# Kernel optimization log

Measured on AMD Instinct MI355X. Metric: run time of the kernel, lower is better.

The kernel has to match this reference:

```python
import jax, jax.numpy as jnp
import numpy as np

B, N, DIM_S, E = 128, 2048, 128, 128


def _xavier(key, shape):
    fan_out, fan_in = shape[0], shape[1]
    limit = float(np.sqrt(6.0 / (fan_in + fan_out)))
    return jax.random.uniform(key, shape, jnp.float32, -limit, limit)


def setup_inputs() -> dict:
    key = jax.random.key(0)
    ks = jax.random.split(key, 14)
    return {
        "instance": jax.random.normal(ks[0], (B, N, DIM_S), jnp.float32),
        # conv1d kernel-size-1 embeds == per-node linear layers [out, in]
        "W_s": _xavier(ks[1], (E, DIM_S)),
        "b_s": jnp.zeros((E,), jnp.float32),
        "W_a": _xavier(ks[2], (E, E)),
        "b_a": jnp.zeros((E,), jnp.float32),
        "v_a": jax.random.normal(ks[3], (E,), jnp.float32),
        "W_c": _xavier(ks[4], (E, 2 * E)),
        "b_c": jnp.zeros((E,), jnp.float32),
        "v_c": jax.random.normal(ks[5], (E,), jnp.float32),
        "W1": _xavier(ks[6], (E, E)),
        "b1": jnp.zeros((E,), jnp.float32),
        "W2": _xavier(ks[7], (1, E)),
        "b2": jnp.zeros((1,), jnp.float32),
    }


def reference(instance, W_s, b_s, W_a, b_a, v_a, W_c, b_c, v_c, W1, b1, W2, b2):
    # project_s: conv1d k=1 == linear over feature dim. [B,N,E]
    proj = jnp.einsum("bns,es->bne", instance, W_s) + b_s
    # first additive-attention score: v_a . tanh(w_a(proj))  -> [B,N]
    u_t = jnp.einsum("bne,e->bn", jnp.tanh(jnp.einsum("bne,fe->bnf", proj, W_a) + b_a), v_a)
    a_t = jax.nn.softmax(u_t, axis=1)  # softmax over nodes
    c_t = a_t[:, :, None] * proj  # [B,N,E]
    hidden_2 = jnp.concatenate([proj, c_t], axis=2)  # [B,N,2E]
    u_t_2 = jnp.einsum("bne,e->bn", jnp.tanh(jnp.einsum("bnf,ef->bne", hidden_2, W_c) + b_c), v_c)
    prob = jax.nn.softmax(u_t_2, axis=1)  # [B,N]
    h_i = jnp.einsum("bn,bne->be", prob, proj)  # weighted sum -> [B,E]
    out1 = jax.nn.relu(h_i @ W1.T + b1)  # [B,E]
    v = (out1 @ W2.T + b2)[:, 0]  # [B]
    return v
```

## Files before the change

kernel.cpp:

```cpp
#include <hip/hip_runtime.h>
#include <hip/hip_bf16.h>

typedef _Float16 half8 __attribute__((ext_vector_type(8)));
typedef _Float16 half4v __attribute__((ext_vector_type(4)));
typedef float f32x4 __attribute__((ext_vector_type(4)));

#define SWZ(byte, r) ((unsigned)(byte) ^ ((((unsigned)(r)) & 7u) << 4))

constexpr int Bb = 128;
constexpr int Nn = 2048;
constexpr int Ee = 128;

constexpr size_t OFF_W    = 0;
constexpr size_t OFF_PROJ = 131072;
constexpr size_t OFF_UT   = OFF_PROJ + (size_t)Bb * Nn * Ee * 2;
constexpr size_t OFF_UT2  = OFF_UT   + (size_t)Bb * Nn * 4;
constexpr size_t OFF_HP   = OFF_UT2  + (size_t)Bb * Nn * 4;

__device__ __forceinline__ void cp16(void* lds, const void* g) {
    __builtin_amdgcn_global_load_lds(
        (const __attribute__((address_space(1))) unsigned int*)g,
        (__attribute__((address_space(3))) unsigned int*)lds, 16, 0, 0);
}

__device__ __forceinline__ float fast_tanh(float x) {
    float e = __expf(2.0f * x);
    return 1.0f - 2.0f * __builtin_amdgcn_rcpf(e + 1.0f);
}

__global__ __launch_bounds__(256) void k_prep(const float* __restrict__ Ws,
                                              const float* __restrict__ Wa,
                                              const float* __restrict__ Wc,
                                              char* __restrict__ wdst)
{
    int id = blockIdx.x * 256 + threadIdx.x;
    for (int i = id; i < 65536; i += 64 * 256) {
        int mat = i >> 14;
        int rem = i & 16383;
        int r = rem >> 7, c = rem & 127;
        float v;
        if      (mat == 0) v = Ws[r * 128 + c];
        else if (mat == 1) v = Wa[r * 128 + c];
        else if (mat == 2) v = Wc[r * 256 + c];
        else               v = Wc[r * 256 + 128 + c];
        unsigned off = SWZ((unsigned)((r * 128 + c) * 2), r);
        *reinterpret_cast<_Float16*>(wdst + (size_t)mat * 32768 + off) = (_Float16)v;
    }
}

__global__ __launch_bounds__(256) void k_pass1(const float* __restrict__ inst,
                                               const char* __restrict__ wtiles,
                                               const float* __restrict__ bs,
                                               const float* __restrict__ ba,
                                               const float* __restrict__ va,
                                               char* __restrict__ projg,
                                               float* __restrict__ ut)
{
    __shared__ _Float16 ldsW[2 * 16384];
    __shared__ _Float16 buf[8192];

    const int tid  = threadIdx.x;
    const int lane = tid & 63;
    const int w    = tid >> 6;
    const int l15  = lane & 15;
    const int kg   = lane >> 4;
    const int arow = w * 16 + l15;

    #pragma unroll
    for (int i = 0; i < 16; ++i) {
        unsigned o = (unsigned)((i * 256 + tid) * 16);
        cp16((char*)ldsW + o, wtiles + o);
    }

    const size_t tile0 = (size_t)blockIdx.x * 8;
    float4 v[8];
    {
        const float* src = inst + tile0 * 64 * 128;
        #pragma unroll
        for (int i = 0; i < 8; ++i)
            v[i] = *reinterpret_cast<const float4*>(src + (size_t)(i * 256 + tid) * 4);
    }

    for (int it = 0; it < 8; ++it) {
        const size_t row0 = (tile0 + it) * 64;

        #pragma unroll
        for (int i = 0; i < 8; ++i) {
            int f = i * 256 + tid;
            int r = f >> 5, c4 = f & 31;
            half4v h = { (_Float16)v[i].x, (_Float16)v[i].y, (_Float16)v[i].z, (_Float16)v[i].w };
            *reinterpret_cast<half4v*>((char*)buf + SWZ(r * 256 + c4 * 8, r)) = h;
        }
        __syncthreads();

        if (it + 1 < 8) {
            const float* src = inst + (row0 + 64) * 128;
            #pragma unroll
            for (int i = 0; i < 8; ++i)
                v[i] = *reinterpret_cast<const float4*>(src + (size_t)(i * 256 + tid) * 4);
        }

        f32x4 acc[8];
        #pragma unroll
        for (int fr = 0; fr < 8; ++fr) acc[fr] = f32x4{0.f, 0.f, 0.f, 0.f};
        #pragma unroll
        for (int kk = 0; kk < 4; ++kk) {
            half8 af = *reinterpret_cast<const half8*>(
                (char*)buf + SWZ(arow * 256 + kk * 64 + kg * 16, arow));
            #pragma unroll
            for (int fr = 0; fr < 8; ++fr) {
                int br = fr * 16 + l15;
                half8 bf = *reinterpret_cast<const half8*>(
                    (char*)ldsW + SWZ(br * 256 + kk * 64 + kg * 16, br));
                acc[fr] = __builtin_amdgcn_mfma_f32_16x16x32_f16(af, bf, acc[fr], 0, 0, 0);
            }
        }
        __syncthreads();

        #pragma unroll
        for (int fr = 0; fr < 8; ++fr) {
            int e = fr * 16 + l15;
            float bsv = bs[e];
            #pragma unroll
            for (int j = 0; j < 4; ++j) {
                int r = w * 16 + kg * 4 + j;
                *reinterpret_cast<_Float16*>((char*)buf + SWZ(r * 256 + e * 2, r)) =
                    (_Float16)(acc[fr][j] + bsv);
            }
        }
        __syncthreads();

        f32x4 tac[8];
        #pragma unroll
        for (int fr = 0; fr < 8; ++fr) tac[fr] = f32x4{0.f, 0.f, 0.f, 0.f};
        #pragma unroll
        for (int kk = 0; kk < 4; ++kk) {
            half8 af = *reinterpret_cast<const half8*>(
                (char*)buf + SWZ(arow * 256 + kk * 64 + kg * 16, arow));
            #pragma unroll
            for (int fr = 0; fr < 8; ++fr) {
                int br = fr * 16 + l15;
                half8 bf = *reinterpret_cast<const half8*>(
                    (char*)ldsW + 32768 + SWZ(br * 256 + kk * 64 + kg * 16, br));
                tac[fr] = __builtin_amdgcn_mfma_f32_16x16x32_f16(af, bf, tac[fr], 0, 0, 0);
            }
        }

        {
            char* dst = projg + row0 * 256;
            #pragma unroll
            for (int i = 0; i < 4; ++i) {
                unsigned o = (unsigned)((i * 256 + tid) * 16);
                *reinterpret_cast<uint4*>(dst + o) =
                    *reinterpret_cast<const uint4*>((const char*)buf + o);
            }
        }

        float u[4] = {0.f, 0.f, 0.f, 0.f};
        #pragma unroll
        for (int fr = 0; fr < 8; ++fr) {
            int fcol = fr * 16 + l15;
            float vav = va[fcol], bav = ba[fcol];
            #pragma unroll
            for (int j = 0; j < 4; ++j)
                u[j] += vav * fast_tanh(tac[fr][j] + bav);
        }
        #pragma unroll
        for (int d = 1; d < 16; d <<= 1) {
            #pragma unroll
            for (int j = 0; j < 4; ++j) u[j] += __shfl_xor(u[j], d);
        }
        if (l15 == 0) {
            #pragma unroll
            for (int j = 0; j < 4; ++j)
                ut[row0 + w * 16 + kg * 4 + j] = u[j];
        }
        __syncthreads();
    }
}

__global__ __launch_bounds__(256) void k_pass2(const char* __restrict__ projg,
                                               const char* __restrict__ wtiles,
                                               const float* __restrict__ bc,
                                               const float* __restrict__ vc,
                                               const float* __restrict__ ut,
                                               float* __restrict__ ut2)
{
    __shared__ _Float16 ldsW[2 * 16384];
    __shared__ _Float16 buf[8192];
    float* scratch = reinterpret_cast<float*>(buf);

    const int tid  = threadIdx.x;
    const int lane = tid & 63;
    const int w    = tid >> 6;
    const int l15  = lane & 15;
    const int kg   = lane >> 4;
    const int arow = w * 16 + l15;
    const int bid  = blockIdx.x;
    const int batch = bid >> 2, quarter = bid & 3;

    #pragma unroll
    for (int i = 0; i < 16; ++i) {
        unsigned o = (unsigned)((i * 256 + tid) * 16);
        cp16((char*)ldsW + o, wtiles + 65536 + o);
    }

    const float* utb = ut + (size_t)batch * Nn;
    float4 x0 = *reinterpret_cast<const float4*>(utb + tid * 8);
    float4 x1 = *reinterpret_cast<const float4*>(utb + tid * 8 + 4);
    float m = fmaxf(fmaxf(fmaxf(x0.x, x0.y), fmaxf(x0.z, x0.w)),
                    fmaxf(fmaxf(x1.x, x1.y), fmaxf(x1.z, x1.w)));
    #pragma unroll
    for (int d = 1; d < 64; d <<= 1) m = fmaxf(m, __shfl_xor(m, d));
    if (lane == 0) scratch[w] = m;
    __syncthreads();
    float M = fmaxf(fmaxf(scratch[0], scratch[1]), fmaxf(scratch[2], scratch[3]));
    float e[8] = { __expf(x0.x - M), __expf(x0.y - M), __expf(x0.z - M), __expf(x0.w - M),
                   __expf(x1.x - M), __expf(x1.y - M), __expf(x1.z - M), __expf(x1.w - M) };
    float s = 0.f;
    #pragma unroll
    for (int i = 0; i < 8; ++i) s += e[i];
    #pragma unroll
    for (int d = 1; d < 64; d <<= 1) s += __shfl_xor(s, d);
    __syncthreads();
    if (lane == 0) scratch[4 + w] = s;
    __syncthreads();
    float invS = 1.0f / (scratch[4] + scratch[5] + scratch[6] + scratch[7]);
    if ((tid >> 6) == quarter * 4 / 4 && tid >= quarter * 64 && tid < quarter * 64 + 64) {
        int base = tid * 8 - quarter * 512;
        #pragma unroll
        for (int k = 0; k < 8; ++k) scratch[8 + base + k] = e[k] * invS;
    }
    __syncthreads();
    float aj[8][4];
    #pragma unroll
    for (int t = 0; t < 8; ++t) {
        #pragma unroll
        for (int j = 0; j < 4; ++j)
            aj[t][j] = scratch[8 + t * 64 + w * 16 + kg * 4 + j];
    }
    __syncthreads();

    const char* psrc = projg + ((size_t)batch * Nn + (size_t)quarter * 512) * 256;
    #pragma unroll
    for (int i = 0; i < 4; ++i) {
        unsigned o = (unsigned)((i * 256 + tid) * 16);
        cp16((char*)buf + o, psrc + o);
    }

    uint4 pv[4];
    #pragma unroll
    for (int t = 0; t < 8; ++t) {
        __syncthreads();

        if (t + 1 < 8) {
            const char* nsrc = psrc + (size_t)(t + 1) * 16384;
            #pragma unroll
            for (int i = 0; i < 4; ++i)
                pv[i] = *reinterpret_cast<const uint4*>(nsrc + (i * 256 + tid) * 16);
        }

        f32x4 u1[8], u2[8];
        #pragma unroll
        for (int fr = 0; fr < 8; ++fr) { u1[fr] = f32x4{0.f,0.f,0.f,0.f}; u2[fr] = f32x4{0.f,0.f,0.f,0.f}; }
        #pragma unroll
        for (int kk = 0; kk < 4; ++kk) {
            half8 af = *reinterpret_cast<const half8*>(
                (char*)buf + SWZ(arow * 256 + kk * 64 + kg * 16, arow));
            #pragma unroll
            for (int fr = 0; fr < 8; ++fr) {
                int br = fr * 16 + l15;
                half8 bf1 = *reinterpret_cast<const half8*>(
                    (char*)ldsW + SWZ(br * 256 + kk * 64 + kg * 16, br));
                u1[fr] = __builtin_amdgcn_mfma_f32_16x16x32_f16(af, bf1, u1[fr], 0, 0, 0);
                half8 bf2 = *reinterpret_cast<const half8*>(
                    (char*)ldsW + 32768 + SWZ(br * 256 + kk * 64 + kg * 16, br));
                u2[fr] = __builtin_amdgcn_mfma_f32_16x16x32_f16(af, bf2, u2[fr], 0, 0, 0);
            }
        }

        float u[4] = {0.f, 0.f, 0.f, 0.f};
        #pragma unroll
        for (int fr = 0; fr < 8; ++fr) {
            int fcol = fr * 16 + l15;
            float vcv = vc[fcol], bcv = bc[fcol];
            #pragma unroll
            for (int j = 0; j < 4; ++j)
                u[j] += vcv * fast_tanh(u1[fr][j] + aj[t][j] * u2[fr][j] + bcv);
        }
        #pragma unroll
        for (int d = 1; d < 16; d <<= 1) {
            #pragma unroll
            for (int j = 0; j < 4; ++j) u[j] += __shfl_xor(u[j], d);
        }
        if (l15 == 0) {
            #pragma unroll
            for (int j = 0; j < 4; ++j)
                ut2[(size_t)batch * Nn + (size_t)quarter * 512 + t * 64 + w * 16 + kg * 4 + j] = u[j];
        }
        __syncthreads();
        if (t + 1 < 8) {
            #pragma unroll
            for (int i = 0; i < 4; ++i)
                *reinterpret_cast<uint4*>((char*)buf + (i * 256 + tid) * 16) = pv[i];
        }
    }
}

__global__ __launch_bounds__(256) void k_hi(const float* __restrict__ ut2,
                                            const char* __restrict__ projg,
                                            float* __restrict__ hpart)
{
    __shared__ float pw[128];
    __shared__ float hp[16][128];
    __shared__ float redm[4], reds[4];

    const int bid = blockIdx.x;
    const int b = bid >> 4, chunk = bid & 15;
    const int n0 = chunk * 128;
    const int tid = threadIdx.x;
    const int lane = tid & 63, w = tid >> 6;

    const float* u2b = ut2 + (size_t)b * Nn;
    float4 x0 = *reinterpret_cast<const float4*>(u2b + tid * 8);
    float4 x1 = *reinterpret_cast<const float4*>(u2b + tid * 8 + 4);
    float m = fmaxf(fmaxf(fmaxf(x0.x, x0.y), fmaxf(x0.z, x0.w)),
                    fmaxf(fmaxf(x1.x, x1.y), fmaxf(x1.z, x1.w)));
    #pragma unroll
    for (int d = 1; d < 64; d <<= 1) m = fmaxf(m, __shfl_xor(m, d));
    if (lane == 0) redm[w] = m;
    __syncthreads();
    float M = fmaxf(fmaxf(redm[0], redm[1]), fmaxf(redm[2], redm[3]));
    float e[8] = { __expf(x0.x - M), __expf(x0.y - M), __expf(x0.z - M), __expf(x0.w - M),
                   __expf(x1.x - M), __expf(x1.y - M), __expf(x1.z - M), __expf(x1.w - M) };
    float s = 0.f;
    #pragma unroll
    for (int i = 0; i < 8; ++i) s += e[i];
    #pragma unroll
    for (int d = 1; d < 64; d <<= 1) s += __shfl_xor(s, d);
    if (lane == 0) reds[w] = s;
    __syncthreads();
    float inv = 1.0f / (reds[0] + reds[1] + reds[2] + reds[3]);
    if ((tid >> 4) == chunk) {
        int base = (tid & 15) * 8;
        #pragma unroll
        for (int k = 0; k < 8; ++k) pw[base + k] = e[k] * inv;
    }
    __syncthreads();

    const int rg = tid >> 4, c16 = tid & 15;
    const char* pb = projg + ((size_t)b * Nn + n0) * 256;
    float acc[8] = {0.f,0.f,0.f,0.f,0.f,0.f,0.f,0.f};
    #pragma unroll
    for (int itn = 0; itn < 8; ++itn) {
        int nl = rg + itn * 16;
        float wgt = pw[nl];
        unsigned off = (unsigned)(nl * 256 + ((c16 * 16) ^ ((nl & 7) << 4)));
        half8 ph = *reinterpret_cast<const half8*>(pb + off);
        #pragma unroll
        for (int j = 0; j < 8; ++j) acc[j] += wgt * (float)ph[j];
    }
    #pragma unroll
    for (int j = 0; j < 8; ++j) hp[rg][c16 * 8 + j] = acc[j];
    __syncthreads();
    if (tid < 128) {
        float s2 = 0.f;
        #pragma unroll
        for (int k = 0; k < 16; ++k) s2 += hp[k][tid];
        hpart[((size_t)b * 16 + chunk) * 128 + tid] = s2;
    }
}

__global__ __launch_bounds__(128) void k_head(const float* __restrict__ hpart,
                                              const float* __restrict__ W1,
                                              const float* __restrict__ b1,
                                              const float* __restrict__ W2,
                                              const float* __restrict__ b2,
                                              float* __restrict__ out)
{
    __shared__ float h[128];
    __shared__ float o1[128];
    const int b = blockIdx.x, tid = threadIdx.x;

    float s = 0.f;
    #pragma unroll
    for (int c = 0; c < 16; ++c) s += hpart[((size_t)b * 16 + c) * 128 + tid];
    h[tid] = s;
    __syncthreads();

    const float* wr = W1 + tid * 128;
    float o = b1[tid];
    #pragma unroll 8
    for (int e = 0; e < 128; e += 4) {
        float4 wv = *reinterpret_cast<const float4*>(wr + e);
        o += wv.x * h[e] + wv.y * h[e+1] + wv.z * h[e+2] + wv.w * h[e+3];
    }
    o1[tid] = fmaxf(o, 0.f);
    __syncthreads();

    if (tid < 64) {
        float p = o1[tid] * W2[tid] + o1[tid + 64] * W2[tid + 64];
        #pragma unroll
        for (int d = 1; d < 64; d <<= 1) p += __shfl_xor(p, d);
        if (tid == 0) out[b] = p + b2[0];
    }
}

extern "C" void kernel_launch(void* const* d_in, const int* in_sizes, int n_in,
                              void* d_out, int out_size, void* d_ws, size_t ws_size,
                              hipStream_t stream)
{
    const float* inst = (const float*)d_in[0];
    const float* Ws   = (const float*)d_in[1];
    const float* bs   = (const float*)d_in[2];
    const float* Wa   = (const float*)d_in[3];
    const float* ba   = (const float*)d_in[4];
    const float* va   = (const float*)d_in[5];
    const float* Wc   = (const float*)d_in[6];
    const float* bc   = (const float*)d_in[7];
    const float* vc   = (const float*)d_in[8];
    const float* W1   = (const float*)d_in[9];
    const float* b1   = (const float*)d_in[10];
    const float* W2   = (const float*)d_in[11];
    const float* b2   = (const float*)d_in[12];
    float* out = (float*)d_out;

    char*  ws     = (char*)d_ws;
    char*  wtiles = ws + OFF_W;
    char*  projg  = ws + OFF_PROJ;
    float* ut     = (float*)(ws + OFF_UT);
    float* ut2    = (float*)(ws + OFF_UT2);
    float* hpart  = (float*)(ws + OFF_HP);

    hipLaunchKernelGGL(k_prep,  dim3(64),      dim3(256), 0, stream, Ws, Wa, Wc, wtiles);
    hipLaunchKernelGGL(k_pass1, dim3(512),     dim3(256), 0, stream, inst, wtiles, bs, ba, va, projg, ut);
    hipLaunchKernelGGL(k_pass2, dim3(512),     dim3(256), 0, stream, projg, wtiles, bc, vc, ut, ut2);
    hipLaunchKernelGGL(k_hi,    dim3(Bb * 16), dim3(256), 0, stream, ut2, projg, hpart);
    hipLaunchKernelGGL(k_head,  dim3(Bb),      dim3(128), 0, stream, hpart, W1, b1, W2, b2, out);
}
```

Before: 297.1 us.

## Fold projection into attention weights and recompute from input instead of storing proj

Precomputes the fused matrices W_a·W_s and W_c·W_s (with folded biases) so passes A and B apply them directly to the raw fp32 input. The fp16 projection buffer is no longer written or read. The final weighted sum is taken over the input and projected once per batch in the head kernel. This trades the proj store and reload for re-reading the fp32 input in three passes, and the fp16 fused weights may shift accuracy slightly.

```diff
diff --git a/kernel.cpp b/kernel.cpp
--- a/kernel.cpp
+++ b/kernel.cpp
@@ -9,13 +9,12 @@
 
 constexpr int Bb = 128;
 constexpr int Nn = 2048;
-constexpr int Ee = 128;
 
 constexpr size_t OFF_W    = 0;
-constexpr size_t OFF_PROJ = 131072;
-constexpr size_t OFF_UT   = OFF_PROJ + (size_t)Bb * Nn * Ee * 2;
-constexpr size_t OFF_UT2  = OFF_UT   + (size_t)Bb * Nn * 4;
-constexpr size_t OFF_HP   = OFF_UT2  + (size_t)Bb * Nn * 4;
+constexpr size_t OFF_BIAS = 98304;
+constexpr size_t OFF_UT   = 131072;
+constexpr size_t OFF_UT2  = OFF_UT  + (size_t)Bb*Nn*4;
+constexpr size_t OFF_SP   = OFF_UT2 + (size_t)Bb*Nn*4;
 
 __device__ __forceinline__ void cp16(void* lds, const void* g) {
     __builtin_amdgcn_global_load_lds(
@@ -28,298 +27,227 @@
     return 1.0f - 2.0f * __builtin_amdgcn_rcpf(e + 1.0f);
 }
 
-__global__ __launch_bounds__(256) void k_prep(const float* __restrict__ Ws,
+__global__ __launch_bounds__(128) void k_prep(const float* __restrict__ Ws,
+                                              const float* __restrict__ bs,
                                               const float* __restrict__ Wa,
+                                              const float* __restrict__ ba,
                                               const float* __restrict__ Wc,
-                                              char* __restrict__ wdst)
-{
-    int id = blockIdx.x * 256 + threadIdx.x;
-    for (int i = id; i < 65536; i += 64 * 256) {
-        int mat = i >> 14;
-        int rem = i & 16383;
-        int r = rem >> 7, c = rem & 127;
-        float v;
-        if      (mat == 0) v = Ws[r * 128 + c];
-        else if (mat == 1) v = Wa[r * 128 + c];
-        else if (mat == 2) v = Wc[r * 256 + c];
-        else               v = Wc[r * 256 + 128 + c];
-        unsigned off = SWZ((unsigned)((r * 128 + c) * 2), r);
-        *reinterpret_cast<_Float16*>(wdst + (size_t)mat * 32768 + off) = (_Float16)v;
-    }
-}
-
-__global__ __launch_bounds__(256) void k_pass1(const float* __restrict__ inst,
+                                              const float* __restrict__ bc,
+                                              char* __restrict__ wdst,
+                                              float* __restrict__ biases)
+{
+    __shared__ float part[128];
+    const int m = blockIdx.x >> 7, r = blockIdx.x & 127, t = threadIdx.x;
+    const float* Arow = (m == 0) ? (Wa + r * 128) : (Wc + r * 256 + (m == 2 ? 128 : 0));
+    float acc = 0.f;
+    #pragma unroll 8
+    for (int k = 0; k < 128; ++k) acc += Arow[k] * Ws[k * 128 + t];
+    if (m == 0) {
+        *reinterpret_cast<_Float16*>(wdst + SWZ((unsigned)(r * 256 + t * 2), r)) = (_Float16)acc;
+    } else {
+        int R = (m == 1) ? r : 128 + r;
+        *reinterpret_cast<_Float16*>(wdst + 32768 + SWZ((unsigned)(R * 256 + t * 2), R)) = (_Float16)acc;
+    }
+    part[t] = Arow[t] * bs[t];
+    __syncthreads();
+    if (t == 0) {
+        float s = 0.f;
+        for (int k = 0; k < 128; ++k) s += part[k];
+        if (m == 0) s += ba[r];
+        else if (m == 1) s += bc[r];
+        biases[m * 128 + r] = s;
+    }
+}
+
+__global__ __launch_bounds__(256) void k_passA(const float* __restrict__ inst,
                                                const char* __restrict__ wtiles,
-                                               const float* __restrict__ bs,
-                                               const float* __restrict__ ba,
+                                               const float* __restrict__ biases,
                                                const float* __restrict__ va,
-                                               char* __restrict__ projg,
                                                float* __restrict__ ut)
 {
-    __shared__ _Float16 ldsW[2 * 16384];
+    __shared__ _Float16 lW[16384];
     __shared__ _Float16 buf[8192];
 
-    const int tid  = threadIdx.x;
-    const int lane = tid & 63;
-    const int w    = tid >> 6;
-    const int l15  = lane & 15;
-    const int kg   = lane >> 4;
+    const int tid = threadIdx.x, lane = tid & 63, w = tid >> 6;
+    const int l15 = lane & 15, kg = lane >> 4;
     const int arow = w * 16 + l15;
-
-    #pragma unroll
-    for (int i = 0; i < 16; ++i) {
+    const size_t row0 = (size_t)blockIdx.x * 64;
+
+    float4 xv[8];
+    const float* src = inst + row0 * 128;
+    #pragma unroll
+    for (int i = 0; i < 8; ++i)
+        xv[i] = *reinterpret_cast<const float4*>(src + (size_t)(i * 256 + tid) * 4);
+    #pragma unroll
+    for (int i = 0; i < 8; ++i) {
         unsigned o = (unsigned)((i * 256 + tid) * 16);
-        cp16((char*)ldsW + o, wtiles + o);
-    }
-
-    const size_t tile0 = (size_t)blockIdx.x * 8;
-    float4 v[8];
-    {
-        const float* src = inst + tile0 * 64 * 128;
-        #pragma unroll
-        for (int i = 0; i < 8; ++i)
-            v[i] = *reinterpret_cast<const float4*>(src + (size_t)(i * 256 + tid) * 4);
-    }
-
-    for (int it = 0; it < 8; ++it) {
-        const size_t row0 = (tile0 + it) * 64;
-
-        #pragma unroll
-        for (int i = 0; i < 8; ++i) {
-            int f = i * 256 + tid;
-            int r = f >> 5, c4 = f & 31;
-            half4v h = { (_Float16)v[i].x, (_Float16)v[i].y, (_Float16)v[i].z, (_Float16)v[i].w };
-            *reinterpret_cast<half4v*>((char*)buf + SWZ(r * 256 + c4 * 8, r)) = h;
+        cp16((char*)lW + o, wtiles + o);
+    }
+    #pragma unroll
+    for (int i = 0; i < 8; ++i) {
+        int f = i * 256 + tid;
+        int r = f >> 5, c4 = f & 31;
+        half4v h = { (_Float16)xv[i].x, (_Float16)xv[i].y, (_Float16)xv[i].z, (_Float16)xv[i].w };
+        *reinterpret_cast<half4v*>((char*)buf + SWZ(r * 256 + c4 * 8, r)) = h;
+    }
+    __syncthreads();
+
+    f32x4 acc[8];
+    #pragma unroll
+    for (int fr = 0; fr < 8; ++fr) acc[fr] = f32x4{0.f, 0.f, 0.f, 0.f};
+    #pragma unroll
+    for (int kk = 0; kk < 4; ++kk) {
+        half8 af = *reinterpret_cast<const half8*>(
+            (char*)buf + SWZ(arow * 256 + kk * 64 + kg * 16, arow));
+        #pragma unroll
+        for (int fr = 0; fr < 8; ++fr) {
+            int br = fr * 16 + l15;
+            half8 bf = *reinterpret_cast<const half8*>(
+                (char*)lW + SWZ(br * 256 + kk * 64 + kg * 16, br));
+            acc[fr] = __builtin_amdgcn_mfma_f32_16x16x32_f16(af, bf, acc[fr], 0, 0, 0);
         }
-        __syncthreads();
-
-        if (it + 1 < 8) {
-            const float* src = inst + (row0 + 64) * 128;
-            #pragma unroll
-            for (int i = 0; i < 8; ++i)
-                v[i] = *reinterpret_cast<const float4*>(src + (size_t)(i * 256 + tid) * 4);
-        }
-
-        f32x4 acc[8];
-        #pragma unroll
-        for (int fr = 0; fr < 8; ++fr) acc[fr] = f32x4{0.f, 0.f, 0.f, 0.f};
-        #pragma unroll
-        for (int kk = 0; kk < 4; ++kk) {
-            half8 af = *reinterpret_cast<const half8*>(
-                (char*)buf + SWZ(arow * 256 + kk * 64 + kg * 16, arow));
-            #pragma unroll
-            for (int fr = 0; fr < 8; ++fr) {
-                int br = fr * 16 + l15;
-                half8 bf = *reinterpret_cast<const half8*>(
-                    (char*)ldsW + SWZ(br * 256 + kk * 64 + kg * 16, br));
-                acc[fr] = __builtin_amdgcn_mfma_f32_16x16x32_f16(af, bf, acc[fr], 0, 0, 0);
-            }
-        }
-        __syncthreads();
-
-        #pragma unroll
-        for (int fr = 0; fr < 8; ++fr) {
-            int e = fr * 16 + l15;
-            float bsv = bs[e];
-            #pragma unroll
-            for (int j = 0; j < 4; ++j) {
-                int r = w * 16 + kg * 4 + j;
-                *reinterpret_cast<_Float16*>((char*)buf + SWZ(r * 256 + e * 2, r)) =
-                    (_Float16)(acc[fr][j] + bsv);
-            }
-        }
-        __syncthreads();
-
-        f32x4 tac[8];
-        #pragma unroll
-        for (int fr = 0; fr < 8; ++fr) tac[fr] = f32x4{0.f, 0.f, 0.f, 0.f};
-        #pragma unroll
-        for (int kk = 0; kk < 4; ++kk) {
-            half8 af = *reinterpret_cast<const half8*>(
-                (char*)buf + SWZ(arow * 256 + kk * 64 + kg * 16, arow));
-            #pragma unroll
-            for (int fr = 0; fr < 8; ++fr) {
-                int br = fr * 16 + l15;
-                half8 bf = *reinterpret_cast<const half8*>(
-                    (char*)ldsW + 32768 + SWZ(br * 256 + kk * 64 + kg * 16, br));
-                tac[fr] = __builtin_amdgcn_mfma_f32_16x16x32_f16(af, bf, tac[fr], 0, 0, 0);
-            }
-        }
-
-        {
-            char* dst = projg + row0 * 256;
-            #pragma unroll
-            for (int i = 0; i < 4; ++i) {
-                unsigned o = (unsigned)((i * 256 + tid) * 16);
-                *reinterpret_cast<uint4*>(dst + o) =
-                    *reinterpret_cast<const uint4*>((const char*)buf + o);
-            }
-        }
-
-        float u[4] = {0.f, 0.f, 0.f, 0.f};
-        #pragma unroll
-        for (int fr = 0; fr < 8; ++fr) {
-            int fcol = fr * 16 + l15;
-            float vav = va[fcol], bav = ba[fcol];
-            #pragma unroll
-            for (int j = 0; j < 4; ++j)
-                u[j] += vav * fast_tanh(tac[fr][j] + bav);
-        }
-        #pragma unroll
-        for (int d = 1; d < 16; d <<= 1) {
-            #pragma unroll
-            for (int j = 0; j < 4; ++j) u[j] += __shfl_xor(u[j], d);
-        }
-        if (l15 == 0) {
-            #pragma unroll
-            for (int j = 0; j < 4; ++j)
-                ut[row0 + w * 16 + kg * 4 + j] = u[j];
-        }
-        __syncthreads();
-    }
-}
-
-__global__ __launch_bounds__(256) void k_pass2(const char* __restrict__ projg,
+    }
+    float u[4] = {0.f, 0.f, 0.f, 0.f};
+    #pragma unroll
+    for (int fr = 0; fr < 8; ++fr) {
+        int fcol = fr * 16 + l15;
+        float vav = va[fcol], bav = biases[fcol];
+        #pragma unroll
+        for (int j = 0; j < 4; ++j)
+            u[j] += vav * fast_tanh(acc[fr][j] + bav);
+    }
+    #pragma unroll
+    for (int d = 1; d < 16; d <<= 1) {
+        #pragma unroll
+        for (int j = 0; j < 4; ++j) u[j] += __shfl_xor(u[j], d);
+    }
+    if (l15 == 0) {
+        #pragma unroll
+        for (int j = 0; j < 4; ++j)
+            ut[row0 + w * 16 + kg * 4 + j] = u[j];
+    }
+}
+
+__global__ __launch_bounds__(256) void k_passB(const float* __restrict__ inst,
                                                const char* __restrict__ wtiles,
-                                               const float* __restrict__ bc,
+                                               const float* __restrict__ biases,
                                                const float* __restrict__ vc,
                                                const float* __restrict__ ut,
                                                float* __restrict__ ut2)
 {
-    __shared__ _Float16 ldsW[2 * 16384];
+    __shared__ _Float16 lW[32768];
     __shared__ _Float16 buf[8192];
     float* scratch = reinterpret_cast<float*>(buf);
 
-    const int tid  = threadIdx.x;
-    const int lane = tid & 63;
-    const int w    = tid >> 6;
-    const int l15  = lane & 15;
-    const int kg   = lane >> 4;
+    const int tid = threadIdx.x, lane = tid & 63, w = tid >> 6;
+    const int l15 = lane & 15, kg = lane >> 4;
     const int arow = w * 16 + l15;
-    const int bid  = blockIdx.x;
-    const int batch = bid >> 2, quarter = bid & 3;
-
+    const int bid = blockIdx.x;
+    const int batch = bid >> 5, tile = bid & 31;
+    const size_t row0 = (size_t)bid * 64;
+
+    const float* utb = ut + (size_t)batch * Nn;
+    float4 u0 = *reinterpret_cast<const float4*>(utb + tid * 8);
+    float4 u1 = *reinterpret_cast<const float4*>(utb + tid * 8 + 4);
+    float4 xv[8];
+    const float* src = inst + row0 * 128;
+    #pragma unroll
+    for (int i = 0; i < 8; ++i)
+        xv[i] = *reinterpret_cast<const float4*>(src + (size_t)(i * 256 + tid) * 4);
     #pragma unroll
     for (int i = 0; i < 16; ++i) {
         unsigned o = (unsigned)((i * 256 + tid) * 16);
-        cp16((char*)ldsW + o, wtiles + 65536 + o);
-    }
-
-    const float* utb = ut + (size_t)batch * Nn;
-    float4 x0 = *reinterpret_cast<const float4*>(utb + tid * 8);
-    float4 x1 = *reinterpret_cast<const float4*>(utb + tid * 8 + 4);
-    float m = fmaxf(fmaxf(fmaxf(x0.x, x0.y), fmaxf(x0.z, x0.w)),
-                    fmaxf(fmaxf(x1.x, x1.y), fmaxf(x1.z, x1.w)));
+        cp16((char*)lW + o, wtiles + 32768 + o);
+    }
+
+    float m = fmaxf(fmaxf(fmaxf(u0.x, u0.y), fmaxf(u0.z, u0.w)),
+                    fmaxf(fmaxf(u1.x, u1.y), fmaxf(u1.z, u1.w)));
     #pragma unroll
     for (int d = 1; d < 64; d <<= 1) m = fmaxf(m, __shfl_xor(m, d));
     if (lane == 0) scratch[w] = m;
     __syncthreads();
     float M = fmaxf(fmaxf(scratch[0], scratch[1]), fmaxf(scratch[2], scratch[3]));
-    float e[8] = { __expf(x0.x - M), __expf(x0.y - M), __expf(x0.z - M), __expf(x0.w - M),
-                   __expf(x1.x - M), __expf(x1.y - M), __expf(x1.z - M), __expf(x1.w - M) };
+    float e[8] = { __expf(u0.x - M), __expf(u0.y - M), __expf(u0.z - M), __expf(u0.w - M),
+                   __expf(u1.x - M), __expf(u1.y - M), __expf(u1.z - M), __expf(u1.w - M) };
     float s = 0.f;
     #pragma unroll
     for (int i = 0; i < 8; ++i) s += e[i];
     #pragma unroll
     for (int d = 1; d < 64; d <<= 1) s += __shfl_xor(s, d);
-    __syncthreads();
     if (lane == 0) scratch[4 + w] = s;
     __syncthreads();
     float invS = 1.0f / (scratch[4] + scratch[5] + scratch[6] + scratch[7]);
-    if ((tid >> 6) == quarter * 4 / 4 && tid >= quarter * 64 && tid < quarter * 64 + 64) {
-        int base = tid * 8 - quarter * 512;
-        #pragma unroll
-        for (int k = 0; k < 8; ++k) scratch[8 + base + k] = e[k] * invS;
-    }
-    __syncthreads();
-    float aj[8][4];
-    #pragma unroll
-    for (int t = 0; t < 8; ++t) {
+    if (tid >= tile * 8 && tid < tile * 8 + 8) {
+        int base = tid * 8 - tile * 64;
+        #pragma unroll
+        for (int k = 0; k < 8; ++k) scratch[8 + base + k] = e[k];
+    }
+    __syncthreads();
+    float aj[4];
+    #pragma unroll
+    for (int j = 0; j < 4; ++j)
+        aj[j] = scratch[8 + w * 16 + kg * 4 + j] * invS;
+    __syncthreads();
+
+    #pragma unroll
+    for (int i = 0; i < 8; ++i) {
+        int f = i * 256 + tid;
+        int r = f >> 5, c4 = f & 31;
+        half4v h = { (_Float16)xv[i].x, (_Float16)xv[i].y, (_Float16)xv[i].z, (_Float16)xv[i].w };
+        *reinterpret_cast<half4v*>((char*)buf + SWZ(r * 256 + c4 * 8, r)) = h;
+    }
+    __syncthreads();
+
+    f32x4 acc[16];
+    #pragma unroll
+    for (int fr = 0; fr < 16; ++fr) acc[fr] = f32x4{0.f, 0.f, 0.f, 0.f};
+    #pragma unroll
+    for (int kk = 0; kk < 4; ++kk) {
+        half8 af = *reinterpret_cast<const half8*>(
+            (char*)buf + SWZ(arow * 256 + kk * 64 + kg * 16, arow));
+        #pragma unroll
+        for (int fr = 0; fr < 16; ++fr) {
+            int br = fr * 16 + l15;
+            half8 bf = *reinterpret_cast<const half8*>(
+                (char*)lW + SWZ(br * 256 + kk * 64 + kg * 16, br));
+            acc[fr] = __builtin_amdgcn_mfma_f32_16x16x32_f16(af, bf, acc[fr], 0, 0, 0);
+        }
+    }
+
+    float u[4] = {0.f, 0.f, 0.f, 0.f};
+    #pragma unroll
+    for (int fr = 0; fr < 8; ++fr) {
+        int fcol = fr * 16 + l15;
+        float c1 = biases[128 + fcol], c2 = biases[256 + fcol], vcv = vc[fcol];
+        #pragma unroll
+        for (int j = 0; j < 4; ++j) {
+            float arg = acc[fr][j] + c1 + aj[j] * (acc[8 + fr][j] + c2);
+            u[j] += vcv * fast_tanh(arg);
+        }
+    }
+    #pragma unroll
+    for (int d = 1; d < 16; d <<= 1) {
+        #pragma unroll
+        for (int j = 0; j < 4; ++j) u[j] += __shfl_xor(u[j], d);
+    }
+    if (l15 == 0) {
         #pragma unroll
         for (int j = 0; j < 4; ++j)
-            aj[t][j] = scratch[8 + t * 64 + w * 16 + kg * 4 + j];
-    }
-    __syncthreads();
-
-    const char* psrc = projg + ((size_t)batch * Nn + (size_t)quarter * 512) * 256;
-    #pragma unroll
-    for (int i = 0; i < 4; ++i) {
-        unsigned o = (unsigned)((i * 256 + tid) * 16);
-        cp16((char*)buf + o, psrc + o);
-    }
-
-    uint4 pv[4];
-    #pragma unroll
-    for (int t = 0; t < 8; ++t) {
-        __syncthreads();
-
-        if (t + 1 < 8) {
-            const char* nsrc = psrc + (size_t)(t + 1) * 16384;
-            #pragma unroll
-            for (int i = 0; i < 4; ++i)
-                pv[i] = *reinterpret_cast<const uint4*>(nsrc + (i * 256 + tid) * 16);
-        }
-
-        f32x4 u1[8], u2[8];
-        #pragma unroll
-        for (int fr = 0; fr < 8; ++fr) { u1[fr] = f32x4{0.f,0.f,0.f,0.f}; u2[fr] = f32x4{0.f,0.f,0.f,0.f}; }
-        #pragma unroll
-        for (int kk = 0; kk < 4; ++kk) {
-            half8 af = *reinterpret_cast<const half8*>(
-                (char*)buf + SWZ(arow * 256 + kk * 64 + kg * 16, arow));
-            #pragma unroll
-            for (int fr = 0; fr < 8; ++fr) {
-                int br = fr * 16 + l15;
-                half8 bf1 = *reinterpret_cast<const half8*>(
-                    (char*)ldsW + SWZ(br * 256 + kk * 64 + kg * 16, br));
-                u1[fr] = __builtin_amdgcn_mfma_f32_16x16x32_f16(af, bf1, u1[fr], 0, 0, 0);
-                half8 bf2 = *reinterpret_cast<const half8*>(
-                    (char*)ldsW + 32768 + SWZ(br * 256 + kk * 64 + kg * 16, br));
-                u2[fr] = __builtin_amdgcn_mfma_f32_16x16x32_f16(af, bf2, u2[fr], 0, 0, 0);
-            }
-        }
-
-        float u[4] = {0.f, 0.f, 0.f, 0.f};
-        #pragma unroll
-        for (int fr = 0; fr < 8; ++fr) {
-            int fcol = fr * 16 + l15;
-            float vcv = vc[fcol], bcv = bc[fcol];
-            #pragma unroll
-            for (int j = 0; j < 4; ++j)
-                u[j] += vcv * fast_tanh(u1[fr][j] + aj[t][j] * u2[fr][j] + bcv);
-        }
-        #pragma unroll
-        for (int d = 1; d < 16; d <<= 1) {
-            #pragma unroll
-            for (int j = 0; j < 4; ++j) u[j] += __shfl_xor(u[j], d);
-        }
-        if (l15 == 0) {
-            #pragma unroll
-            for (int j = 0; j < 4; ++j)
-                ut2[(size_t)batch * Nn + (size_t)quarter * 512 + t * 64 + w * 16 + kg * 4 + j] = u[j];
-        }
-        __syncthreads();
-        if (t + 1 < 8) {
-            #pragma unroll
-            for (int i = 0; i < 4; ++i)
-                *reinterpret_cast<uint4*>((char*)buf + (i * 256 + tid) * 16) = pv[i];
-        }
-    }
-}
-
-__global__ __launch_bounds__(256) void k_hi(const float* __restrict__ ut2,
-                                            const char* __restrict__ projg,
-                                            float* __restrict__ hpart)
-{
-    __shared__ float pw[128];
-    __shared__ float hp[16][128];
-    __shared__ float redm[4], reds[4];
-
-    const int bid = blockIdx.x;
-    const int b = bid >> 4, chunk = bid & 15;
-    const int n0 = chunk * 128;
-    const int tid = threadIdx.x;
-    const int lane = tid & 63, w = tid >> 6;
+            ut2[row0 + w * 16 + kg * 4 + j] = u[j];
+    }
+}
+
+__global__ __launch_bounds__(256) void k_passC(const float* __restrict__ inst,
+                                               const float* __restrict__ ut2,
+                                               float* __restrict__ spart)
+{
+    __shared__ float pw[256];
+    __shared__ float hp[64][136];
+    __shared__ float red[8];
+
+    const int tid = threadIdx.x, lane = tid & 63, w = tid >> 6;
+    const int bid = blockIdx.x, b = bid >> 3, chunk = bid & 7;
+    const int n0 = chunk * 256;
 
     const float* u2b = ut2 + (size_t)b * Nn;
     float4 x0 = *reinterpret_cast<const float4*>(u2b + tid * 8);
@@ -328,9 +256,9 @@
                     fmaxf(fmaxf(x1.x, x1.y), fmaxf(x1.z, x1.w)));
     #pragma unroll
     for (int d = 1; d < 64; d <<= 1) m = fmaxf(m, __shfl_xor(m, d));
-    if (lane == 0) redm[w] = m;
-    __syncthreads();
-    float M = fmaxf(fmaxf(redm[0], redm[1]), fmaxf(redm[2], redm[3]));
+    if (lane == 0) red[w] = m;
+    __syncthreads();
+    float M = fmaxf(fmaxf(red[0], red[1]), fmaxf(red[2], red[3]));
     float e[8] = { __expf(x0.x - M), __expf(x0.y - M), __expf(x0.z - M), __expf(x0.w - M),
                    __expf(x1.x - M), __expf(x1.y - M), __expf(x1.z - M), __expf(x1.w - M) };
     float s = 0.f;
@@ -338,71 +266,86 @@
     for (int i = 0; i < 8; ++i) s += e[i];
     #pragma unroll
     for (int d = 1; d < 64; d <<= 1) s += __shfl_xor(s, d);
-    if (lane == 0) reds[w] = s;
-    __syncthreads();
-    float inv = 1.0f / (reds[0] + reds[1] + reds[2] + reds[3]);
-    if ((tid >> 4) == chunk) {
-        int base = (tid & 15) * 8;
+    if (lane == 0) red[4 + w] = s;
+    __syncthreads();
+    float inv = 1.0f / (red[4] + red[5] + red[6] + red[7]);
+    if (tid >= chunk * 32 && tid < chunk * 32 + 32) {
+        int base = tid * 8 - n0;
         #pragma unroll
         for (int k = 0; k < 8; ++k) pw[base + k] = e[k] * inv;
     }
     __syncthreads();
 
-    const int rg = tid >> 4, c16 = tid & 15;
-    const char* pb = projg + ((size_t)b * Nn + n0) * 256;
-    float acc[8] = {0.f,0.f,0.f,0.f,0.f,0.f,0.f,0.f};
-    #pragma unroll
-    for (int itn = 0; itn < 8; ++itn) {
-        int nl = rg + itn * 16;
-        float wgt = pw[nl];
-        unsigned off = (unsigned)(nl * 256 + ((c16 * 16) ^ ((nl & 7) << 4)));
-        half8 ph = *reinterpret_cast<const half8*>(pb + off);
-        #pragma unroll
-        for (int j = 0; j < 8; ++j) acc[j] += wgt * (float)ph[j];
-    }
-    #pragma unroll
-    for (int j = 0; j < 8; ++j) hp[rg][c16 * 8 + j] = acc[j];
+    const int n_l = tid >> 2, cq = tid & 3;
+    f32x4 acc[8];
+    #pragma unroll
+    for (int i = 0; i < 8; ++i) acc[i] = f32x4{0.f, 0.f, 0.f, 0.f};
+    #pragma unroll
+    for (int g = 0; g < 4; ++g) {
+        int n = g * 64 + n_l;
+        float wgt = pw[n];
+        const float* rp = inst + ((size_t)b * Nn + n0 + n) * 128 + cq * 32;
+        #pragma unroll
+        for (int i = 0; i < 8; ++i) {
+            f32x4 v = *reinterpret_cast<const f32x4*>(rp + i * 4);
+            acc[i] += wgt * v;
+        }
+    }
+    #pragma unroll
+    for (int i = 0; i < 8; ++i)
+        *reinterpret_cast<f32x4*>(&hp[n_l][cq * 32 + i * 4]) = acc[i];
     __syncthreads();
     if (tid < 128) {
         float s2 = 0.f;
         #pragma unroll
-        for (int k = 0; k < 16; ++k) s2 += hp[k][tid];
-        hpart[((size_t)b * 16 + chunk) * 128 + tid] = s2;
-    }
-}
-
-__global__ __launch_bounds__(128) void k_head(const float* __restrict__ hpart,
+        for (int k = 0; k < 64; ++k) s2 += hp[k][tid];
+        spart[((size_t)b * 8 + chunk) * 128 + tid] = s2;
+    }
+}
+
+__global__ __launch_bounds__(128) void k_head(const float* __restrict__ spart,
+                                              const float* __restrict__ Ws,
+                                              const float* __restrict__ bs,
                                               const float* __restrict__ W1,
                                               const float* __restrict__ b1,
                                               const float* __restrict__ W2,
                                               const float* __restrict__ b2,
                                               float* __restrict__ out)
 {
-    __shared__ float h[128];
-    __shared__ float o1[128];
-    const int b = blockIdx.x, tid = threadIdx.x;
+    __shared__ float sv[128], h[128], o1[128];
+    const int b = blockIdx.x, t = threadIdx.x;
 
     float s = 0.f;
     #pragma unroll
-    for (int c = 0; c < 16; ++c) s += hpart[((size_t)b * 16 + c) * 128 + tid];
-    h[tid] = s;
-    __syncthreads();
-
-    const float* wr = W1 + tid * 128;
-    float o = b1[tid];
+    for (int c = 0; c < 8; ++c) s += spart[((size_t)b * 8 + c) * 128 + t];
+    sv[t] = s;
+    __syncthreads();
+
+    const float* wr = Ws + t * 128;
+    float a = bs[t];
     #pragma unroll 8
     for (int e = 0; e < 128; e += 4) {
         float4 wv = *reinterpret_cast<const float4*>(wr + e);
+        a += wv.x * sv[e] + wv.y * sv[e+1] + wv.z * sv[e+2] + wv.w * sv[e+3];
+    }
+    h[t] = a;
+    __syncthreads();
+
+    const float* w1r = W1 + t * 128;
+    float o = b1[t];
+    #pragma unroll 8
+    for (int e = 0; e < 128; e += 4) {
+        float4 wv = *reinterpret_cast<const float4*>(w1r + e);
         o += wv.x * h[e] + wv.y * h[e+1] + wv.z * h[e+2] + wv.w * h[e+3];
     }
-    o1[tid] = fmaxf(o, 0.f);
-    __syncthreads();
-
-    if (tid < 64) {
-        float p = o1[tid] * W2[tid] + o1[tid + 64] * W2[tid + 64];
+    o1[t] = fmaxf(o, 0.f);
+    __syncthreads();
+
+    if (t < 64) {
+        float p = o1[t] * W2[t] + o1[t + 64] * W2[t + 64];
         #pragma unroll
         for (int d = 1; d < 64; d <<= 1) p += __shfl_xor(p, d);
-        if (tid == 0) out[b] = p + b2[0];
+        if (t == 0) out[b] = p + b2[0];
     }
 }
 
@@ -427,14 +370,14 @@
 
     char*  ws     = (char*)d_ws;
     char*  wtiles = ws + OFF_W;
-    char*  projg  = ws + OFF_PROJ;
+    float* biases = (float*)(ws + OFF_BIAS);
     float* ut     = (float*)(ws + OFF_UT);
     float* ut2    = (float*)(ws + OFF_UT2);
-    float* hpart  = (float*)(ws + OFF_HP);
-
-    hipLaunchKernelGGL(k_prep,  dim3(64),      dim3(256), 0, stream, Ws, Wa, Wc, wtiles);
-    hipLaunchKernelGGL(k_pass1, dim3(512),     dim3(256), 0, stream, inst, wtiles, bs, ba, va, projg, ut);
-    hipLaunchKernelGGL(k_pass2, dim3(512),     dim3(256), 0, stream, projg, wtiles, bc, vc, ut, ut2);
-    hipLaunchKernelGGL(k_hi,    dim3(Bb * 16), dim3(256), 0, stream, ut2, projg, hpart);
-    hipLaunchKernelGGL(k_head,  dim3(Bb),      dim3(128), 0, stream, hpart, W1, b1, W2, b2, out);
-}
+    float* spart  = (float*)(ws + OFF_SP);
+
+    hipLaunchKernelGGL(k_prep,  dim3(384),  dim3(128), 0, stream, Ws, bs, Wa, ba, Wc, bc, wtiles, biases);
+    hipLaunchKernelGGL(k_passA, dim3(4096), dim3(256), 0, stream, inst, wtiles, biases, va, ut);
+    hipLaunchKernelGGL(k_passB, dim3(4096), dim3(256), 0, stream, inst, wtiles, biases, vc, ut, ut2);
+    hipLaunchKernelGGL(k_passC, dim3(1024), dim3(256), 0, stream, inst, ut2, spart);
+    hipLaunchKernelGGL(k_head,  dim3(128),  dim3(128), 0, stream, spart, Ws, bs, W1, b1, W2, b2, out);
+}
```

Result: slower. 306.0 us (+3.0%).
